# Performance work log

Measured on AMD Instinct MI355X. Metric: run time of the kernel, lower is better.

## Reference

```python
import jax, jax.numpy as jnp
import numpy as np

B, L, D, H, FF = 2, 2048, 1024, 16, 4096
DH = D // H
EPS = 1e-5  # torch LayerNorm default


def _layernorm(x, g, b):
    mu = jnp.mean(x, axis=-1, keepdims=True)
    var = jnp.mean(jnp.square(x - mu), axis=-1, keepdims=True)
    return (x - mu) * jax.lax.rsqrt(var + EPS) * g + b


def setup_inputs() -> dict:
    key = jax.random.key(0)
    ks = jax.random.split(key, 8)
    s = 0.02  # typical init scale for weights
    return {
        "x": jax.random.normal(ks[0], (B, L, D), jnp.float32),
        "pos_embed": jax.random.normal(ks[1], (1, L, D), jnp.float32) * s,
        "ln1_g": jnp.ones((D,), jnp.float32),
        "ln1_b": jnp.zeros((D,), jnp.float32),
        "Wq": jax.random.normal(ks[2], (D, D), jnp.float32) * s,
        "Wk": jax.random.normal(ks[3], (D, D), jnp.float32) * s,
        "Wv": jax.random.normal(ks[4], (D, D), jnp.float32) * s,
        "Wo": jax.random.normal(ks[5], (D, D), jnp.float32) * s,
        "bo": jnp.zeros((D,), jnp.float32),
        "ln2_g": jnp.ones((D,), jnp.float32),
        "ln2_b": jnp.zeros((D,), jnp.float32),
        "W1": jax.random.normal(ks[6], (D, FF), jnp.float32) * s,
        "b1": jnp.zeros((FF,), jnp.float32),
        "W2": jax.random.normal(ks[7], (FF, D), jnp.float32) * s,
        "b2": jnp.zeros((D,), jnp.float32),
    }


def reference(x, pos_embed, ln1_g, ln1_b, Wq, Wk, Wv, Wo, bo, ln2_g, ln2_b, W1, b1, W2, b2):
    scale = DH ** -0.5
    residual = x
    h = _layernorm(x, ln1_g, ln1_b) + pos_embed  # [B,L,D]
    # qkv projections (no bias, qkv_bias=False default), split into heads
    q = (h @ Wq).reshape(B, L, H, DH).transpose(0, 2, 1, 3)  # [B,H,L,DH]
    k = (h @ Wk).reshape(B, L, H, DH).transpose(0, 2, 1, 3)
    v = (h @ Wv).reshape(B, L, H, DH).transpose(0, 2, 1, 3)
    attn = jnp.einsum("bhqd,bhkd->bhqk", q, k) * scale  # [B,H,L,L]
    attn = jax.nn.softmax(attn, axis=-1)
    out = jnp.einsum("bhqk,bhkd->bhqd", attn, v)  # [B,H,L,DH]
    out = out.transpose(0, 2, 1, 3).reshape(B, L, D)
    out = out @ Wo + bo
    x = residual + out
    # MLP with pre-norm
    m = _layernorm(x, ln2_g, ln2_b)
    m = jax.nn.gelu(m @ W1 + b1, approximate=False) @ W2 + b2
    return x + m
```

## Files before the change

kernel.cpp:

```cpp
#include <hip/hip_runtime.h>
#include <hip/hip_bf16.h>
#include <cstdint>

typedef __bf16 bf16_t;
typedef __bf16 bf16x8 __attribute__((ext_vector_type(8)));
typedef __bf16 bf16x4v __attribute__((ext_vector_type(4)));
typedef short s16x4 __attribute__((ext_vector_type(4)));
typedef float f32x4 __attribute__((ext_vector_type(4)));

#define B_ 2
#define L_ 2048
#define D_ 1024
#define H_ 16
#define DH_ 64
#define FF_ 4096
#define M_TOT (B_*L_)

#define CLOG2 0.18033688011112042f


__device__ __forceinline__ void gload_lds16(const void* g, void* l) {
    __builtin_amdgcn_global_load_lds((__attribute__((address_space(1))) void*)g,
                                     (__attribute__((address_space(3))) void*)l,
                                     16, 0, 0);
}

__device__ __forceinline__ float fast_exp2(float v) {
    return __builtin_amdgcn_exp2f(v);
}

__device__ __forceinline__ float gelu_fast(float x) {
    float x3 = x * x * x;
    float y  = fmaf(0.044715f, x3, x);
    float e  = fast_exp2(y * 2.3022213f);
    float t  = fmaf(-2.0f, __builtin_amdgcn_rcpf(e + 1.0f), 1.0f);
    return 0.5f * x * (1.0f + t);
}

__global__ void transpose_bf16_kernel(const float* __restrict__ W, bf16_t* __restrict__ WT,
                                      int K, int N) {
    __shared__ float t[32][33];
    int tx = threadIdx.x, ty = threadIdx.y;
    int n0 = blockIdx.x * 32, k0 = blockIdx.y * 32;
#pragma unroll
    for (int i = 0; i < 4; i++)
        t[ty + 8 * i][tx] = W[(size_t)(k0 + ty + 8 * i) * N + n0 + tx];
    __syncthreads();
#pragma unroll
    for (int i = 0; i < 4; i++)
        WT[(size_t)(n0 + ty + 8 * i) * K + k0 + tx] = (bf16_t)t[tx][ty + 8 * i];
}

__global__ void transpose_qkvo_kernel(const float* __restrict__ Wq, const float* __restrict__ Wk,
                                      const float* __restrict__ Wv, const float* __restrict__ Wo,
                                      bf16_t* __restrict__ WqkvT, bf16_t* __restrict__ WoT) {
    int z = blockIdx.z;
    const float* W = (z == 0) ? Wq : (z == 1) ? Wk : (z == 2) ? Wv : Wo;
    bf16_t* dst = (z < 3) ? (WqkvT + (size_t)z * 1024 * 1024) : WoT;
    __shared__ float t[32][33];
    int tx = threadIdx.x, ty = threadIdx.y;
    int n0 = blockIdx.x * 32, k0 = blockIdx.y * 32;
#pragma unroll
    for (int i = 0; i < 4; i++)
        t[ty + 8 * i][tx] = W[(size_t)(k0 + ty + 8 * i) * D_ + n0 + tx];
    __syncthreads();
#pragma unroll
    for (int i = 0; i < 4; i++)
        dst[(size_t)(n0 + ty + 8 * i) * D_ + k0 + tx] = (bf16_t)t[tx][ty + 8 * i];
}

__global__ __launch_bounds__(256) void ln_kernel(const float* __restrict__ x,
                                                 const float* __restrict__ pos,
                                                 const float* __restrict__ g,
                                                 const float* __restrict__ beta,
                                                 bf16_t* __restrict__ out) {
    int row = blockIdx.x, tid = threadIdx.x;
    const float* xr = x + (size_t)row * D_;
    float v[4];
    float s = 0.f, sq = 0.f;
#pragma unroll
    for (int i = 0; i < 4; i++) {
        float a = xr[tid + 256 * i];
        v[i] = a; s += a; sq += a * a;
    }
#pragma unroll
    for (int o = 32; o > 0; o >>= 1) { s += __shfl_xor(s, o); sq += __shfl_xor(sq, o); }
    __shared__ float red[8];
    int wid = tid >> 6;
    if ((tid & 63) == 0) { red[wid] = s; red[4 + wid] = sq; }
    __syncthreads();
    s  = red[0] + red[1] + red[2] + red[3];
    sq = red[4] + red[5] + red[6] + red[7];
    float mu  = s * (1.f / D_);
    float var = sq * (1.f / D_) - mu * mu;
    float rs  = rsqrtf(var + 1e-5f);
    int l = row & (L_ - 1);
#pragma unroll
    for (int i = 0; i < 4; i++) {
        int c = tid + 256 * i;
        float hv = (v[i] - mu) * rs * g[c] + beta[c];
        if (pos) hv += pos[(size_t)l * D_ + c];
        out[(size_t)row * D_ + c] = (bf16_t)hv;
    }
}

__global__ __launch_bounds__(256) void addbias_kernel(const float* __restrict__ src,
                                                      const float* __restrict__ bias,
                                                      float* __restrict__ dst) {
    int i = (blockIdx.x * 256 + threadIdx.x) * 4;
    float4 v = *(const float4*)(src + i);
    float4 bv = *(const float4*)(bias + (i & (D_ - 1)));
    v.x += bv.x; v.y += bv.y; v.z += bv.z; v.w += bv.w;
    *(float4*)(dst + i) = v;
}

template <int EPI, typename OutT>
__global__ __launch_bounds__(256) void gemm_kernel(const bf16_t* __restrict__ A,
                                                   const bf16_t* __restrict__ BT,
                                                   OutT* __restrict__ C,
                                                   const float* __restrict__ bias,
                                                   bf16_t* __restrict__ Vt,
                                                   int M, int N, int K) {
    __shared__ __align__(16) bf16_t sA[2][128 * 32];
    __shared__ __align__(16) bf16_t sB[2][128 * 32];
    int tid = threadIdx.x;
    int lane = tid & 63, w = tid >> 6, wy = w >> 1, wx = w & 1;
    int qm = lane & 15, quad = lane >> 4;
    int row0 = blockIdx.x * 128, col0 = blockIdx.y * 128;
    f32x4 acc[4][4] = {};
    int sf[2], sra[2], scol[2];
#pragma unroll
    for (int c = 0; c < 2; c++) {
        int f = tid * 8 + c * 2048;
        sf[c] = f;
        sra[c] = f >> 5;
        int ch = (f >> 3) & 3;
        scol[c] = ((ch ^ ((sra[c] >> 1) & 3)) << 3);
    }
    int aoff[4], boff[4];
#pragma unroll
    for (int t = 0; t < 4; t++) {
        int Ra = wy * 64 + t * 16 + qm;
        int Rb = wx * 64 + t * 16 + qm;
        aoff[t] = Ra * 32 + ((quad ^ ((Ra >> 1) & 3)) << 3);
        boff[t] = Rb * 32 + ((quad ^ ((Rb >> 1) & 3)) << 3);
    }
    const bf16_t* Ab = A  + (size_t)row0 * K;
    const bf16_t* Bb = BT + (size_t)col0 * K;
#pragma unroll
    for (int c = 0; c < 2; c++) {
        gload_lds16(Ab + (size_t)sra[c] * K + scol[c], &sA[0][sf[c]]);
        gload_lds16(Bb + (size_t)sra[c] * K + scol[c], &sB[0][sf[c]]);
    }
    for (int k0 = 0; k0 < K; k0 += 32) {
        int cur = (k0 >> 5) & 1;
        __syncthreads();
        int kn = k0 + 32;
        if (kn < K) {
#pragma unroll
            for (int c = 0; c < 2; c++) {
                gload_lds16(Ab + (size_t)sra[c] * K + kn + scol[c], &sA[cur ^ 1][sf[c]]);
                gload_lds16(Bb + (size_t)sra[c] * K + kn + scol[c], &sB[cur ^ 1][sf[c]]);
            }
        }
        bf16x8 af[4], bfr[4];
#pragma unroll
        for (int mt = 0; mt < 4; mt++) af[mt] = *(const bf16x8*)&sA[cur][aoff[mt]];
#pragma unroll
        for (int nt = 0; nt < 4; nt++) bfr[nt] = *(const bf16x8*)&sB[cur][boff[nt]];
#pragma unroll
        for (int mt = 0; mt < 4; mt++)
#pragma unroll
            for (int nt = 0; nt < 4; nt++)
                acc[mt][nt] = __builtin_amdgcn_mfma_f32_16x16x32_bf16(af[mt], bfr[nt],
                                                                      acc[mt][nt], 0, 0, 0);
    }
    if (EPI == 4 && col0 >= 2048) {
#pragma unroll
        for (int mt = 0; mt < 4; mt++) {
            int row_base = row0 + wy * 64 + mt * 16 + quad * 4;
            int bb = row_base >> 11, key0 = row_base & 2047;
#pragma unroll
            for (int nt = 0; nt < 4; nt++) {
                int vcol = col0 - 2048 + wx * 64 + nt * 16 + qm;
                int hh = vcol >> 6, dd = vcol & 63;
                bf16x4v pk;
#pragma unroll
                for (int r = 0; r < 4; r++) pk[r] = (bf16_t)acc[mt][nt][r];
                *(bf16x4v*)&Vt[(size_t)(((bb << 4) + hh) * 64 + dd) * 2048 + key0] = pk;
            }
        }
        return;
    }
    float qscale = (EPI == 4 && col0 < 1024) ? CLOG2 : 1.0f;
#pragma unroll
    for (int mt = 0; mt < 4; mt++) {
#pragma unroll
        for (int nt = 0; nt < 4; nt++) {
            int col = col0 + wx * 64 + nt * 16 + qm;
#pragma unroll
            for (int r = 0; r < 4; r++) {
                int row = row0 + wy * 64 + mt * 16 + quad * 4 + r;
                float v = acc[mt][nt][r];
                if (EPI == 2) { v += bias[col]; v = gelu_fast(v); }
                if (EPI == 4) C[(size_t)row * 2048 + col] = (OutT)(v * qscale);
                else          C[(size_t)row * N + col] = (OutT)v;
            }
        }
    }
}

__global__ __launch_bounds__(256) void gemm_splitk_kernel(const bf16_t* __restrict__ A,
                                                          const bf16_t* __restrict__ BT,
                                                          float* __restrict__ C,
                                                          int N, int Ktot, int Ksplit) {
    __shared__ __align__(16) bf16_t sA[2][128 * 32];
    __shared__ __align__(16) bf16_t sB[2][128 * 32];
    int tid = threadIdx.x;
    int lane = tid & 63, w = tid >> 6, wy = w >> 1, wx = w & 1;
    int qm = lane & 15, quad = lane >> 4;
    int row0 = blockIdx.x * 128, col0 = blockIdx.y * 128;
    size_t koff = (size_t)blockIdx.z * Ksplit;
    f32x4 acc[4][4] = {};
    int sf[2], sra[2], scol[2];
#pragma unroll
    for (int c = 0; c < 2; c++) {
        int f = tid * 8 + c * 2048;
        sf[c] = f;
        sra[c] = f >> 5;
        int ch = (f >> 3) & 3;
        scol[c] = ((ch ^ ((sra[c] >> 1) & 3)) << 3);
    }
    int aoff[4], boff[4];
#pragma unroll
    for (int t = 0; t < 4; t++) {
        int Ra = wy * 64 + t * 16 + qm;
        int Rb = wx * 64 + t * 16 + qm;
        aoff[t] = Ra * 32 + ((quad ^ ((Ra >> 1) & 3)) << 3);
        boff[t] = Rb * 32 + ((quad ^ ((Rb >> 1) & 3)) << 3);
    }
    const bf16_t* Ab = A  + (size_t)row0 * Ktot + koff;
    const bf16_t* Bb = BT + (size_t)col0 * Ktot + koff;
#pragma unroll
    for (int c = 0; c < 2; c++) {
        gload_lds16(Ab + (size_t)sra[c] * Ktot + scol[c], &sA[0][sf[c]]);
        gload_lds16(Bb + (size_t)sra[c] * Ktot + scol[c], &sB[0][sf[c]]);
    }
    for (int k0 = 0; k0 < Ksplit; k0 += 32) {
        int cur = (k0 >> 5) & 1;
        __syncthreads();
        int kn = k0 + 32;
        if (kn < Ksplit) {
#pragma unroll
            for (int c = 0; c < 2; c++) {
                gload_lds16(Ab + (size_t)sra[c] * Ktot + kn + scol[c], &sA[cur ^ 1][sf[c]]);
                gload_lds16(Bb + (size_t)sra[c] * Ktot + kn + scol[c], &sB[cur ^ 1][sf[c]]);
            }
        }
        bf16x8 af[4], bfr[4];
#pragma unroll
        for (int mt = 0; mt < 4; mt++) af[mt] = *(const bf16x8*)&sA[cur][aoff[mt]];
#pragma unroll
        for (int nt = 0; nt < 4; nt++) bfr[nt] = *(const bf16x8*)&sB[cur][boff[nt]];
#pragma unroll
        for (int mt = 0; mt < 4; mt++)
#pragma unroll
            for (int nt = 0; nt < 4; nt++)
                acc[mt][nt] = __builtin_amdgcn_mfma_f32_16x16x32_bf16(af[mt], bfr[nt],
                                                                      acc[mt][nt], 0, 0, 0);
    }
#pragma unroll
    for (int mt = 0; mt < 4; mt++) {
#pragma unroll
        for (int nt = 0; nt < 4; nt++) {
            int col = col0 + wx * 64 + nt * 16 + qm;
#pragma unroll
            for (int r = 0; r < 4; r++) {
                int row = row0 + wy * 64 + mt * 16 + quad * 4 + r;
                atomicAdd(&C[(size_t)row * N + col], acc[mt][nt][r]);
            }
        }
    }
}

__global__ __launch_bounds__(256) void attn_kernel(const bf16_t* __restrict__ QK,
                                                   const bf16_t* __restrict__ Vt,
                                                   bf16_t* __restrict__ O) {
    __shared__ __align__(16) bf16_t sK[2][64 * 64];
    __shared__ __align__(16) bf16_t sV[2][64 * 64];
    int tid = threadIdx.x, lane = tid & 63, w = tid >> 6;
    int qm = lane & 15, quad = lane >> 4;
    int q0 = blockIdx.x * 128 + w * 32;
    int bh = blockIdx.y, b = bh >> 4, h = bh & 15;

    const bf16_t* Qbase = QK + (size_t)(b * L_) * 2048 + h * 64;
    const bf16_t* Kbase = Qbase + 1024;
    const bf16_t* Vbase = Vt + (size_t)bh * 64 * 2048;

    bf16x8 qf[2][2];
#pragma unroll
    for (int g = 0; g < 2; g++) {
        const bf16_t* qp = Qbase + (size_t)(q0 + g * 16 + qm) * 2048 + quad * 8;
        qf[g][0] = *(const bf16x8*)qp;
        qf[g][1] = *(const bf16x8*)(qp + 32);
    }

    int f0 = tid * 8, f1 = f0 + 2048;
    int r0 = f0 >> 6, sc0 = ((((f0 >> 3) & 7) ^ (r0 & 7)) << 3);
    int r1 = f1 >> 6, sc1 = ((((f1 >> 3) & 7) ^ (r1 & 7)) << 3);

    gload_lds16(Kbase + (size_t)r0 * 2048 + sc0, &sK[0][f0]);
    gload_lds16(Kbase + (size_t)r1 * 2048 + sc1, &sK[0][f1]);
    gload_lds16(Vbase + (size_t)r0 * 2048 + sc0, &sV[0][f0]);
    gload_lds16(Vbase + (size_t)r1 * 2048 + sc1, &sV[0][f1]);

    f32x4 o[2][4] = {};
    float l_[2] = {0.f, 0.f};

    int kfo[4][2], vfo[4][4];
#pragma unroll
    for (int kt = 0; kt < 4; kt++) {
#pragma unroll
        for (int ks = 0; ks < 2; ks++) {
            int row = kt * 16 + qm;
            kfo[kt][ks] = row * 64 + ((((ks << 2) + quad) ^ (row & 7)) << 3);
        }
#pragma unroll
        for (int dt = 0; dt < 4; dt++) {
            int row = dt * 16 + qm;
            int cw = (kt << 1) + (quad >> 1);
            vfo[dt][kt] = row * 64 + ((cw ^ (row & 7)) << 3) + ((quad & 1) << 2);
        }
    }

    for (int kv0 = 0; kv0 < L_; kv0 += 64) {
        int cur = (kv0 >> 6) & 1;
        __syncthreads();
        int kn = kv0 + 64;
        if (kn < L_) {
            gload_lds16(Kbase + (size_t)(kn + r0) * 2048 + sc0, &sK[cur ^ 1][f0]);
            gload_lds16(Kbase + (size_t)(kn + r1) * 2048 + sc1, &sK[cur ^ 1][f1]);
            gload_lds16(Vbase + (size_t)r0 * 2048 + kn + sc0, &sV[cur ^ 1][f0]);
            gload_lds16(Vbase + (size_t)r1 * 2048 + kn + sc1, &sV[cur ^ 1][f1]);
        }

        bf16x8 kf[4][2];
#pragma unroll
        for (int kt = 0; kt < 4; kt++)
#pragma unroll
            for (int ks = 0; ks < 2; ks++)
                kf[kt][ks] = *(const bf16x8*)&sK[cur][kfo[kt][ks]];
        f32x4 s[2][4] = {};
#pragma unroll
        for (int kt = 0; kt < 4; kt++)
#pragma unroll
            for (int ks = 0; ks < 2; ks++) {
                s[0][kt] = __builtin_amdgcn_mfma_f32_16x16x32_bf16(kf[kt][ks], qf[0][ks], s[0][kt], 0, 0, 0);
                s[1][kt] = __builtin_amdgcn_mfma_f32_16x16x32_bf16(kf[kt][ks], qf[1][ks], s[1][kt], 0, 0, 0);
            }

        s16x4 pf[2][4];
#pragma unroll
        for (int g = 0; g < 2; g++) {
            float sum = l_[g];
#pragma unroll
            for (int kt = 0; kt < 4; kt++) {
                union { bf16x4v b; s16x4 i; } u;
#pragma unroll
                for (int r = 0; r < 4; r++) {
                    float p = fast_exp2(s[g][kt][r]);
                    sum += p;
                    u.b[r] = (bf16_t)p;
                }
                pf[g][kt] = u.i;
            }
            l_[g] = sum;
        }

#pragma unroll
        for (int dt = 0; dt < 4; dt++)
#pragma unroll
            for (int kt = 0; kt < 4; kt++) {
                s16x4 vf = *(const s16x4*)&sV[cur][vfo[dt][kt]];
                o[0][dt] = __builtin_amdgcn_mfma_f32_16x16x16bf16_1k(vf, pf[0][kt], o[0][dt], 0, 0, 0);
                o[1][dt] = __builtin_amdgcn_mfma_f32_16x16x16bf16_1k(vf, pf[1][kt], o[1][dt], 0, 0, 0);
            }
    }

#pragma unroll
    for (int g = 0; g < 2; g++) {
        float lt = l_[g];
        lt += __shfl_xor(lt, 16);
        lt += __shfl_xor(lt, 32);
        float rl = 1.0f / lt;
        size_t row = (size_t)(b * L_ + q0 + g * 16 + qm);
#pragma unroll
        for (int dt = 0; dt < 4; dt++) {
            bf16x4v pk;
#pragma unroll
            for (int r = 0; r < 4; r++) pk[r] = (bf16_t)(o[g][dt][r] * rl);
            *(bf16x4v*)&O[row * D_ + h * 64 + dt * 16 + quad * 4] = pk;
        }
    }
}


extern "C" void kernel_launch(void* const* d_in, const int* in_sizes, int n_in,
                              void* d_out, int out_size, void* d_ws, size_t ws_size,
                              hipStream_t stream) {
    const float* x   = (const float*)d_in[0];
    const float* pos = (const float*)d_in[1];
    const float* g1  = (const float*)d_in[2];
    const float* be1 = (const float*)d_in[3];
    const float* Wq  = (const float*)d_in[4];
    const float* Wk  = (const float*)d_in[5];
    const float* Wv  = (const float*)d_in[6];
    const float* Wo  = (const float*)d_in[7];
    const float* bo  = (const float*)d_in[8];
    const float* g2  = (const float*)d_in[9];
    const float* be2 = (const float*)d_in[10];
    const float* W1  = (const float*)d_in[11];
    const float* b1m = (const float*)d_in[12];
    const float* W2  = (const float*)d_in[13];
    const float* b2m = (const float*)d_in[14];

    char* ws = (char*)d_ws;
    const size_t MB = 1ull << 20;
    bf16_t* W2T   = (bf16_t*)(ws + 0);
    float*  x2    = (float*) (ws + 8 * MB);
    bf16_t* ff1   = (bf16_t*)(ws + 24 * MB);
    bf16_t* qk    = (bf16_t*)(ws + 24 * MB);
    bf16_t* Vt    = (bf16_t*)(ws + 40 * MB);
    bf16_t* hb    = (bf16_t*)(ws + 48 * MB);
    bf16_t* attnO = (bf16_t*)(ws + 56 * MB);
    bf16_t* mb    = (bf16_t*)(ws + 56 * MB);
    bf16_t* W1T   = (bf16_t*)(ws + 64 * MB);
    bf16_t* WqkvT = (bf16_t*)(ws + 72 * MB);
    bf16_t* WoT   = (bf16_t*)(ws + 78 * MB);

    dim3 tb(32, 8);
    transpose_qkvo_kernel<<<dim3(32, 32, 4), tb, 0, stream>>>(Wq, Wk, Wv, Wo, WqkvT, WoT);
    transpose_bf16_kernel<<<dim3(128, 32), tb, 0, stream>>>(W1, W1T, D_, FF_);
    transpose_bf16_kernel<<<dim3(32, 128), tb, 0, stream>>>(W2, W2T, FF_, D_);

    ln_kernel<<<M_TOT, 256, 0, stream>>>(x, pos, g1, be1, hb);

    gemm_kernel<4, bf16_t><<<dim3(32, 24), 256, 0, stream>>>(hb, WqkvT, qk, nullptr,
                                                             Vt, M_TOT, 3072, D_);

    attn_kernel<<<dim3(16, 32), 256, 0, stream>>>(qk, Vt, attnO);

    addbias_kernel<<<M_TOT * D_ / 1024, 256, 0, stream>>>(x, bo, x2);
    gemm_splitk_kernel<<<dim3(32, 8, 4), 256, 0, stream>>>(attnO, WoT, x2,
                                                           D_, D_, D_ / 4);

    ln_kernel<<<M_TOT, 256, 0, stream>>>(x2, nullptr, g2, be2, mb);

    addbias_kernel<<<M_TOT * D_ / 1024, 256, 0, stream>>>(x2, b2m, (float*)d_out);

    gemm_kernel<2, bf16_t><<<dim3(32, 32), 256, 0, stream>>>(mb, W1T, ff1, b1m,
                                                             nullptr, M_TOT, FF_, D_);

    gemm_splitk_kernel<<<dim3(32, 8, 4), 256, 0, stream>>>(ff1, W2T, (float*)d_out,
                                                           D_, FF_, FF_ / 4);

    (void)in_sizes; (void)n_in; (void)out_size; (void)ws_size;
}
```

Baseline: 442.4 us.

## Replace atomic split-K with 2-way partial stores fused into LN and output reduction

The Wo and W2 split-K GEMMs now use 2 splits instead of 4 and write their partial sums to separate buffers with plain stores instead of atomicAdd. The residual, bias and partial-sum reduction for the attention output is folded into a new fused LayerNorm kernel. The final output is formed by a reduce kernel that adds x2, b2 and both partials. This drops the two addbias passes and the float atomics, at the cost of extra partial-buffer traffic, half as many blocks in the split-K launches, and workspace regions reused for the partials.

New measurement: 370.6 us. 16.2% less time.

```diff
diff --git a/kernel.cpp b/kernel.cpp
--- a/kernel.cpp
+++ b/kernel.cpp
@@ -104,14 +104,57 @@
     }
 }
 
-__global__ __launch_bounds__(256) void addbias_kernel(const float* __restrict__ src,
-                                                      const float* __restrict__ bias,
-                                                      float* __restrict__ dst) {
+__global__ __launch_bounds__(256) void ln_fuse_kernel(const float* __restrict__ x,
+                                                      const float* __restrict__ bo,
+                                                      const float* __restrict__ P0,
+                                                      const float* __restrict__ P1,
+                                                      const float* __restrict__ g,
+                                                      const float* __restrict__ beta,
+                                                      float* __restrict__ x2,
+                                                      bf16_t* __restrict__ out) {
+    int row = blockIdx.x, tid = threadIdx.x;
+    size_t base = (size_t)row * D_;
+    float v[4];
+    float s = 0.f, sq = 0.f;
+#pragma unroll
+    for (int i = 0; i < 4; i++) {
+        int c = tid + 256 * i;
+        float a = x[base + c] + bo[c] + P0[base + c] + P1[base + c];
+        v[i] = a; s += a; sq += a * a;
+        x2[base + c] = a;
+    }
+#pragma unroll
+    for (int o = 32; o > 0; o >>= 1) { s += __shfl_xor(s, o); sq += __shfl_xor(sq, o); }
+    __shared__ float red[8];
+    int wid = tid >> 6;
+    if ((tid & 63) == 0) { red[wid] = s; red[4 + wid] = sq; }
+    __syncthreads();
+    s  = red[0] + red[1] + red[2] + red[3];
+    sq = red[4] + red[5] + red[6] + red[7];
+    float mu  = s * (1.f / D_);
+    float var = sq * (1.f / D_) - mu * mu;
+    float rs  = rsqrtf(var + 1e-5f);
+#pragma unroll
+    for (int i = 0; i < 4; i++) {
+        int c = tid + 256 * i;
+        out[base + c] = (bf16_t)((v[i] - mu) * rs * g[c] + beta[c]);
+    }
+}
+
+__global__ __launch_bounds__(256) void reduce_out_kernel(const float* __restrict__ x2,
+                                                         const float* __restrict__ bias,
+                                                         const float* __restrict__ P1,
+                                                         float* __restrict__ dout) {
     int i = (blockIdx.x * 256 + threadIdx.x) * 4;
-    float4 v = *(const float4*)(src + i);
+    float4 a  = *(const float4*)(x2 + i);
     float4 bv = *(const float4*)(bias + (i & (D_ - 1)));
-    v.x += bv.x; v.y += bv.y; v.z += bv.z; v.w += bv.w;
-    *(float4*)(dst + i) = v;
+    float4 p0 = *(const float4*)(dout + i);
+    float4 p1 = *(const float4*)(P1 + i);
+    a.x += bv.x + p0.x + p1.x;
+    a.y += bv.y + p0.y + p1.y;
+    a.z += bv.z + p0.z + p1.z;
+    a.w += bv.w + p0.w + p1.w;
+    *(float4*)(dout + i) = a;
 }
 
 template <int EPI, typename OutT>
@@ -210,10 +253,11 @@
     }
 }
 
-__global__ __launch_bounds__(256) void gemm_splitk_kernel(const bf16_t* __restrict__ A,
-                                                          const bf16_t* __restrict__ BT,
-                                                          float* __restrict__ C,
-                                                          int N, int Ktot, int Ksplit) {
+__global__ __launch_bounds__(256) void gemm_splitk_st_kernel(const bf16_t* __restrict__ A,
+                                                             const bf16_t* __restrict__ BT,
+                                                             float* __restrict__ P0,
+                                                             float* __restrict__ P1,
+                                                             int N, int Ktot, int Ksplit) {
     __shared__ __align__(16) bf16_t sA[2][128 * 32];
     __shared__ __align__(16) bf16_t sB[2][128 * 32];
     int tid = threadIdx.x;
@@ -269,6 +313,7 @@
                 acc[mt][nt] = __builtin_amdgcn_mfma_f32_16x16x32_bf16(af[mt], bfr[nt],
                                                                       acc[mt][nt], 0, 0, 0);
     }
+    float* P = blockIdx.z ? P1 : P0;
 #pragma unroll
     for (int mt = 0; mt < 4; mt++) {
 #pragma unroll
@@ -277,7 +322,7 @@
 #pragma unroll
             for (int r = 0; r < 4; r++) {
                 int row = row0 + wy * 64 + mt * 16 + quad * 4 + r;
-                atomicAdd(&C[(size_t)row * N + col], acc[mt][nt][r]);
+                P[(size_t)row * N + col] = acc[mt][nt][r];
             }
         }
     }
@@ -428,13 +473,16 @@
     const size_t MB = 1ull << 20;
     bf16_t* W2T   = (bf16_t*)(ws + 0);
     float*  x2    = (float*) (ws + 8 * MB);
-    bf16_t* ff1   = (bf16_t*)(ws + 24 * MB);
     bf16_t* qk    = (bf16_t*)(ws + 24 * MB);
     bf16_t* Vt    = (bf16_t*)(ws + 40 * MB);
     bf16_t* hb    = (bf16_t*)(ws + 48 * MB);
+    float*  Pwo0  = (float*) (ws + 24 * MB);
+    float*  Pwo1  = (float*) (ws + 40 * MB);
     bf16_t* attnO = (bf16_t*)(ws + 56 * MB);
     bf16_t* mb    = (bf16_t*)(ws + 56 * MB);
+    bf16_t* ff1   = (bf16_t*)(ws + 24 * MB);
     bf16_t* W1T   = (bf16_t*)(ws + 64 * MB);
+    float*  Pff1  = (float*) (ws + 56 * MB);
     bf16_t* WqkvT = (bf16_t*)(ws + 72 * MB);
     bf16_t* WoT   = (bf16_t*)(ws + 78 * MB);
 
@@ -450,19 +498,18 @@
 
     attn_kernel<<<dim3(16, 32), 256, 0, stream>>>(qk, Vt, attnO);
 
-    addbias_kernel<<<M_TOT * D_ / 1024, 256, 0, stream>>>(x, bo, x2);
-    gemm_splitk_kernel<<<dim3(32, 8, 4), 256, 0, stream>>>(attnO, WoT, x2,
-                                                           D_, D_, D_ / 4);
-
-    ln_kernel<<<M_TOT, 256, 0, stream>>>(x2, nullptr, g2, be2, mb);
-
-    addbias_kernel<<<M_TOT * D_ / 1024, 256, 0, stream>>>(x2, b2m, (float*)d_out);
+    gemm_splitk_st_kernel<<<dim3(32, 8, 2), 256, 0, stream>>>(attnO, WoT, Pwo0, Pwo1,
+                                                              D_, D_, D_ / 2);
+
+    ln_fuse_kernel<<<M_TOT, 256, 0, stream>>>(x, bo, Pwo0, Pwo1, g2, be2, x2, mb);
 
     gemm_kernel<2, bf16_t><<<dim3(32, 32), 256, 0, stream>>>(mb, W1T, ff1, b1m,
                                                              nullptr, M_TOT, FF_, D_);
 
-    gemm_splitk_kernel<<<dim3(32, 8, 4), 256, 0, stream>>>(ff1, W2T, (float*)d_out,
-                                                           D_, FF_, FF_ / 4);
+    gemm_splitk_st_kernel<<<dim3(32, 8, 2), 256, 0, stream>>>(ff1, W2T, (float*)d_out,
+                                                              Pff1, D_, FF_, FF_ / 2);
+
+    reduce_out_kernel<<<M_TOT * D_ / 1024, 256, 0, stream>>>(x2, b2m, Pff1, (float*)d_out);
 
     (void)in_sizes; (void)n_in; (void)out_size; (void)ws_size;
 }
```
